# Kernel optimization log

Hardware: AMD Instinct MI355X
Metric: run time of the kernel (lower is better)

Reference implementation:

```python
import jax, jax.numpy as jnp
import numpy as np

B, L, IN, OUT = 32, 2048, 192, 2
H, N2, NL = 512, 32, 4  # hidden_dim, d_state//2 complex modes, num_layers


def setup_inputs() -> dict:
    key = jax.random.key(0)
    ks = jax.random.split(key, 8)
    neural_input = jax.random.normal(ks[0], (B, L, IN), jnp.float32)
    W_in = jax.random.normal(ks[1], (IN, H), jnp.float32) / np.sqrt(IN)
    b_in = jnp.zeros((H,), jnp.float32)
    # S4D kernel params (stacked over layers)
    log_dt = jax.random.uniform(ks[2], (NL, H), jnp.float32, np.log(1e-3), np.log(1e-1))
    Cri = jax.random.normal(ks[3], (NL, H, N2, 2), jnp.float32)  # complex C as (re, im)
    log_A_real = jnp.full((NL, H, N2), np.log(0.5), jnp.float32)
    A_imag = jnp.broadcast_to(np.pi * jnp.arange(N2, dtype=np.float32), (NL, H, N2)).astype(jnp.float32)
    D = jax.random.normal(ks[4], (NL, H), jnp.float32)
    # position-wise output conv1x1 producing 2H channels for GLU
    conv_w = jax.random.normal(ks[5], (NL, 2 * H, H), jnp.float32) / np.sqrt(H)
    conv_b = jnp.zeros((NL, 2 * H), jnp.float32)
    W_out = jax.random.normal(ks[6], (H, OUT), jnp.float32) / np.sqrt(H)
    b_out = jnp.zeros((OUT,), jnp.float32)
    return dict(neural_input=neural_input, W_in=W_in, b_in=b_in, log_dt=log_dt,
                Cri=Cri, log_A_real=log_A_real, A_imag=A_imag, D=D,
                conv_w=conv_w, conv_b=conv_b, W_out=W_out, b_out=b_out)


def _s4d_layer(u, log_dt, Cri, log_A_real, A_imag, D, conv_w, conv_b):
    # u: (B, H, L)
    Lx = u.shape[-1]
    dt = jnp.exp(log_dt)[:, None]                       # (H, 1)
    C = Cri[..., 0] + 1j * Cri[..., 1]                  # (H, N2) complex
    A = -jnp.exp(log_A_real) + 1j * A_imag              # (H, N2)
    dtA = A * dt                                        # (H, N2)
    Ct = C * (jnp.exp(dtA) - 1.0) / A                   # (H, N2)
    # Vandermonde kernel: K[h, l] = 2 Re sum_n Ct[h,n] exp(dtA[h,n] * l)
    vand = jnp.exp(dtA[..., None] * jnp.arange(Lx))     # (H, N2, L) complex
    K = 2.0 * jnp.einsum('hn,hnl->hl', Ct, vand).real   # (H, L)
    # circular conv via FFT at length 2L (== linear conv, causal)
    k_f = jnp.fft.rfft(K, n=2 * Lx)
    u_f = jnp.fft.rfft(u, n=2 * Lx)
    y = jnp.fft.irfft(u_f * k_f, n=2 * Lx)[..., :Lx]    # (B, H, L)
    y = y + u * D[:, None]
    y = jax.nn.gelu(y, approximate=False)               # torch nn.GELU (erf)
    # conv1x1 to 2H channels + GLU over channel dim
    z = jnp.einsum('oh,bhl->bol', conv_w, y) + conv_b[None, :, None]
    a, b = jnp.split(z, 2, axis=1)
    return a * jax.nn.sigmoid(b)


def reference(neural_input, W_in, b_in, log_dt, Cri, log_A_real, A_imag, D,
              conv_w, conv_b, W_out, b_out):
    x = neural_input @ W_in + b_in          # (B, L, H)
    u = jnp.transpose(x, (0, 2, 1))         # (B, H, L) channels-first for SSM
    for i in range(NL):
        u = _s4d_layer(u, log_dt[i], Cri[i], log_A_real[i], A_imag[i],
                       D[i], conv_w[i], conv_b[i])
    y = jnp.transpose(u, (0, 2, 1))         # (B, L, H)
    return y @ W_out + b_out                # (B, L, OUT)
```

## Files before the change

kernel.cpp:

```cpp
#include <hip/hip_runtime.h>
#include <hip/hip_bf16.h>
#include <math.h>

#define BB 32
#define LL 2048
#define INP 192
#define OUTC 2
#define HH 512
#define NN2 32
#define NNL 4
#define TABB 32768

using short8 = __attribute__((ext_vector_type(8))) short;
using f32x4  = __attribute__((ext_vector_type(4))) float;
using f32x2  = __attribute__((ext_vector_type(2))) float;

struct u2x2 { uint2 a, b; };

__device__ __forceinline__ float sigmoidf_(float x) {
  return 1.0f / (1.0f + expf(-x));
}
__device__ __forceinline__ unsigned short bf16bits(float x) {
  __hip_bfloat16 b = __float2bfloat16(x);
  return __builtin_bit_cast(unsigned short, b);
}
__device__ __forceinline__ float bfval(unsigned short b) {
  unsigned int u = (unsigned int)b << 16;
  return __builtin_bit_cast(float, u);
}
__device__ __forceinline__ unsigned packsplit(float v) {
  unsigned short hb = bf16bits(v);
  unsigned short lb = bf16bits(v - bfval(hb));
  return ((unsigned)hb << 16) | (unsigned)lb;
}
__device__ __forceinline__ float gelu_fast(float x) {
  float s = x * 0.70710678118654752f;
  float ax = fabsf(s);
  float tt = 1.0f / fmaf(0.3275911f, ax, 1.0f);
  float p = fmaf(1.061405429f, tt, -1.453152027f);
  p = fmaf(p, tt, 1.421413741f);
  p = fmaf(p, tt, -0.284496736f);
  p = fmaf(p, tt, 0.254829592f);
  float e = __expf(-s * s);
  float er = 1.0f - p * tt * e;
  er = copysignf(er, s);
  return 0.5f * x * (1.0f + er);
}
__device__ __forceinline__ void gload16(const void* gsrc, void* ldst) {
  __builtin_amdgcn_global_load_lds(
      (const __attribute__((address_space(1))) void*)gsrc,
      (__attribute__((address_space(3))) void*)ldst, 16, 0, 0);
}

__global__ __launch_bounds__(256) void k_params(const float* __restrict__ log_dt,
                                                const float* __restrict__ Cri,
                                                const float* __restrict__ lAr,
                                                const float* __restrict__ Aim,
                                                float* __restrict__ P) {
  int idx = blockIdx.x * 256 + threadIdx.x;
  if (idx >= NNL * HH * NN2) return;
  float dt  = expf(log_dt[idx / NN2]);
  float Are = -expf(lAr[idx]);
  float Aimv = Aim[idx];
  float dre = Are * dt, dim = Aimv * dt;
  float er = expf(dre);
  float wrv = er * cosf(dim);
  float wiv = er * sinf(dim);
  float Er = wrv - 1.0f, Ei = wiv;
  float den = Are * Are + Aimv * Aimv;
  float Fr = (Er * Are + Ei * Aimv) / den;
  float Fi = (Ei * Are - Er * Aimv) / den;
  float Cre = Cri[idx * 2 + 0], Cim = Cri[idx * 2 + 1];
  P[idx * 4 + 0] = wrv;
  P[idx * 4 + 1] = wiv;
  P[idx * 4 + 2] = 2.0f * (Cre * Fr - Cim * Fi);
  P[idx * 4 + 3] = 2.0f * (Cre * Fi + Cim * Fr);
}

__global__ __launch_bounds__(64) void k_tables(const float* __restrict__ P,
                                               const float* __restrict__ Dp,
                                               char* __restrict__ Tab) {
  __shared__ float kk[32];
  int tid = threadIdx.x;
  int lh = blockIdx.x;
  char* tb = Tab + (size_t)lh * TABB;
  if (tid < 32) {
    int n = tid;
    const float4 pq = reinterpret_cast<const float4*>(P)[(size_t)lh * NN2 + n];
    float wr = pq.x, wi = pq.y, c2r = pq.z, c2i = pq.w;
    int mt = n >> 4;
    float pr = 1.0f, pi = 0.0f;
    for (int d = 0; d < 32; ++d) {
      {
        int t_ = 31 - d;
        int lane = ((t_ >> 3) << 4) + (n & 15);
        int j = t_ & 7;
        unsigned short hr = bf16bits(pr);
        unsigned short lr = bf16bits(pr - bfval(hr));
        unsigned short hi_ = bf16bits(pi);
        unsigned short li_ = bf16bits(pi - bfval(hi_));
        *(unsigned short*)(tb + (mt * 2 + 0) * 1024 + lane * 16 + j * 2) = hr;
        *(unsigned short*)(tb + (mt * 2 + 1) * 1024 + lane * 16 + j * 2) = hi_;
        *(unsigned short*)(tb + 4096 + (mt * 2 + 0) * 1024 + lane * 16 + j * 2) = lr;
        *(unsigned short*)(tb + 4096 + (mt * 2 + 1) * 1024 + lane * 16 + j * 2) = li_;
      }
      {
        int mtT = d >> 4;
        int lane = (((n & 15) >> 2) << 4) + (d & 15);
        int jre = n & 3, jim = (n & 3) + 4;
        unsigned short hr = bf16bits(pr);
        unsigned short lr = bf16bits(pr - bfval(hr));
        float nim = -pi;
        unsigned short hi_ = bf16bits(nim);
        unsigned short li_ = bf16bits(nim - bfval(hi_));
        char* bh = tb + 8192 + (mtT * 2 + mt) * 1024 + lane * 16;
        char* bl = tb + 12288 + (mtT * 2 + mt) * 1024 + lane * 16;
        *(unsigned short*)(bh + jre * 2) = hr;
        *(unsigned short*)(bh + jim * 2) = hi_;
        *(unsigned short*)(bl + jre * 2) = lr;
        *(unsigned short*)(bl + jim * 2) = li_;
      }
      float kp = c2r * pr - c2i * pi;
      #pragma unroll
      for (int k = 1; k < 32; k <<= 1) kp += __shfl_xor(kp, k, 32);
      if (n == 0) kk[d] = (d == 0) ? (kp + Dp[lh]) : kp;
      float nr = pr * wr - pi * wi;
      pi = pr * wi + pi * wr;
      pr = nr;
    }
    float w32r = pr, w32i = pi;
    float c2wr = c2r * wr - c2i * wi;
    float c2wi = c2r * wi + c2i * wr;
    int s = ((n >> 4) << 2) + (n & 3);
    int gg = (n & 15) >> 2;
    float pmr = 1.0f, pmi = 0.0f;
    for (int m = 0; m < 16; ++m) {
      float* q = (float*)(tb + 20480 + (size_t)((s * 64) + (gg * 16 + m)) * 24);
      q[0] = w32r; q[1] = w32i; q[2] = pmr; q[3] = pmi; q[4] = c2wr; q[5] = c2wi;
      float t2 = pmr * w32r - pmi * w32i;
      pmi = pmr * w32i + pmi * w32r;
      pmr = t2;
    }
  }
  __syncthreads();
  for (int idx = tid; idx < 1024; idx += 64) {
    int mt = idx >> 9, rem = idx & 511;
    int lane = rem >> 3, j = rem & 7;
    int tt = (mt << 4) + (lane & 15);
    int jf = ((lane >> 4) << 3) + j;
    float val = (jf <= tt) ? kk[tt - jf] : 0.0f;
    unsigned short hb = bf16bits(val);
    unsigned short lb = bf16bits(val - bfval(hb));
    *(unsigned short*)(tb + 16384 + mt * 1024 + lane * 16 + j * 2) = hb;
    *(unsigned short*)(tb + 18432 + mt * 1024 + lane * 16 + j * 2) = lb;
  }
}

__global__ __launch_bounds__(256) void k_tobf16(const float* __restrict__ src,
                                                __hip_bfloat16* __restrict__ dst,
                                                int n) {
  int i = (blockIdx.x * 256 + threadIdx.x) * 4;
  if (i >= n) return;
  float4 v = *reinterpret_cast<const float4*>(&src[i]);
  dst[i + 0] = __float2bfloat16(v.x);
  dst[i + 1] = __float2bfloat16(v.y);
  dst[i + 2] = __float2bfloat16(v.z);
  dst[i + 3] = __float2bfloat16(v.w);
}

__global__ __launch_bounds__(256) void k_splitx(const float* __restrict__ src,
                                                __hip_bfloat16* __restrict__ hi,
                                                __hip_bfloat16* __restrict__ lo,
                                                int n) {
  int i = (blockIdx.x * 256 + threadIdx.x) * 4;
  if (i >= n) return;
  float4 v = *reinterpret_cast<const float4*>(&src[i]);
  float vv[4] = {v.x, v.y, v.z, v.w};
  unsigned short hb[4], lb[4];
  #pragma unroll
  for (int j = 0; j < 4; ++j) {
    hb[j] = bf16bits(vv[j]);
    lb[j] = bf16bits(vv[j] - bfval(hb[j]));
  }
  *reinterpret_cast<uint2*>(hi + i) = make_uint2(
      (unsigned)hb[0] | ((unsigned)hb[1] << 16), (unsigned)hb[2] | ((unsigned)hb[3] << 16));
  *reinterpret_cast<uint2*>(lo + i) = make_uint2(
      (unsigned)lb[0] | ((unsigned)lb[1] << 16), (unsigned)lb[2] | ((unsigned)lb[3] << 16));
}

__global__ __launch_bounds__(256) void k_prepwt(const float* __restrict__ W,
                                                __hip_bfloat16* __restrict__ hi,
                                                __hip_bfloat16* __restrict__ lo) {
  int idx = blockIdx.x * 256 + threadIdx.x;
  if (idx >= HH * INP) return;
  int h = idx / INP, k = idx - h * INP;
  float v = W[(size_t)k * HH + h];
  unsigned short hb = bf16bits(v);
  hi[idx] = __builtin_bit_cast(__hip_bfloat16, hb);
  lo[idx] = __float2bfloat16(v - bfval(hb));
}

__global__ __launch_bounds__(256) void k_ingemm(const __hip_bfloat16* __restrict__ Xhi,
                                                const __hip_bfloat16* __restrict__ Xlo,
                                                const __hip_bfloat16* __restrict__ Wthi,
                                                const __hip_bfloat16* __restrict__ Wtlo,
                                                const float* __restrict__ bias,
                                                unsigned* __restrict__ Upk) {
  int lt = blockIdx.x * 128;
  int ht = blockIdx.y * 128;
  int b  = blockIdx.z;
  int t = threadIdx.x;
  int wid = t >> 6, lane = t & 63;
  int wrow = wid >> 1, wcol = wid & 1;
  int l15 = lane & 15, g = lane >> 4;

  const short* Xh = (const short*)Xhi + (size_t)b * LL * INP;
  const short* Xl = (const short*)Xlo + (size_t)b * LL * INP;
  const short* Bh = (const short*)Wthi;
  const short* Bl = (const short*)Wtlo;

  f32x4 acc[4][4];
  #pragma unroll
  for (int m = 0; m < 4; ++m)
    #pragma unroll
    for (int n = 0; n < 4; ++n) acc[m][n] = f32x4{0.f, 0.f, 0.f, 0.f};

  int lbase = lt + wrow * 64 + l15;
  int hbase = ht + wcol * 64 + l15;

  #pragma unroll
  for (int ks = 0; ks < 6; ++ks) {
    int k0 = ks * 32 + 8 * g;
    short8 ah[4], al[4], bh[4], bl[4];
    #pragma unroll
    for (int m = 0; m < 4; ++m) {
      size_t off = (size_t)(lbase + m * 16) * INP + k0;
      ah[m] = *reinterpret_cast<const short8*>(Xh + off);
      al[m] = *reinterpret_cast<const short8*>(Xl + off);
    }
    #pragma unroll
    for (int n = 0; n < 4; ++n) {
      size_t off = (size_t)(hbase + n * 16) * INP + k0;
      bh[n] = *reinterpret_cast<const short8*>(Bh + off);
      bl[n] = *reinterpret_cast<const short8*>(Bl + off);
    }
    #pragma unroll
    for (int m = 0; m < 4; ++m)
      #pragma unroll
      for (int n = 0; n < 4; ++n) {
        acc[m][n] = __builtin_amdgcn_mfma_f32_16x16x32_bf16(ah[m], bh[n], acc[m][n], 0, 0, 0);
        acc[m][n] = __builtin_amdgcn_mfma_f32_16x16x32_bf16(ah[m], bl[n], acc[m][n], 0, 0, 0);
        acc[m][n] = __builtin_amdgcn_mfma_f32_16x16x32_bf16(al[m], bh[n], acc[m][n], 0, 0, 0);
      }
  }

  #pragma unroll
  for (int n = 0; n < 4; ++n) {
    int h = hbase + n * 16;
    float bv = bias[h];
    size_t rowoff = ((size_t)b * HH + h) * LL;
    #pragma unroll
    for (int m = 0; m < 4; ++m) {
      int l0 = lt + wrow * 64 + m * 16 + g * 4;
      uint4 o;
      o.x = packsplit(acc[m][n][0] + bv);
      o.y = packsplit(acc[m][n][1] + bv);
      o.z = packsplit(acc[m][n][2] + bv);
      o.w = packsplit(acc[m][n][3] + bv);
      *reinterpret_cast<uint4*>(Upk + rowoff + l0) = o;
    }
  }
}

__global__ __launch_bounds__(256) void k_scan(const unsigned* __restrict__ Upk,
                                              short* __restrict__ Ybt,
                                              const char* __restrict__ Tab) {
  __shared__ __align__(16) char smem[16384];
  int t = threadIdx.x;
  int lane = t & 63;
  int wid = t >> 6;
  int row = __builtin_amdgcn_readfirstlane(blockIdx.x * 4 + wid);
  int h = row & (HH - 1);
  const char* tb = Tab + (size_t)h * TABB;
  const unsigned* urow = Upk + (size_t)row * LL;
  int g = lane >> 4, m = lane & 15;

  short8 uh[4], ul[4];
  #pragma unroll
  for (int c0 = 0; c0 < 4; ++c0) {
    int off = 512 * c0 + 32 * m + 8 * g;
    uint4 pa = *reinterpret_cast<const uint4*>(urow + off);
    uint4 pb = *reinterpret_cast<const uint4*>(urow + off + 4);
    unsigned p[8] = {pa.x, pa.y, pa.z, pa.w, pb.x, pb.y, pb.z, pb.w};
    unsigned hw[4], lw[4];
    #pragma unroll
    for (int w = 0; w < 4; ++w) {
      unsigned p0 = p[2 * w], p1 = p[2 * w + 1];
      hw[w] = (p1 & 0xFFFF0000u) | (p0 >> 16);
      lw[w] = (p1 << 16) | (p0 & 0x0000FFFFu);
    }
    uh[c0] = __builtin_bit_cast(short8, make_uint4(hw[0], hw[1], hw[2], hw[3]));
    ul[c0] = __builtin_bit_cast(short8, make_uint4(lw[0], lw[1], lw[2], lw[3]));
  }

  short8 afh[2][4], afl[2][4];
  #pragma unroll
  for (int mt = 0; mt < 2; ++mt) {
    f32x4 Z[2][4];
    #pragma unroll
    for (int reim = 0; reim < 2; ++reim) {
      short8 whi = *reinterpret_cast<const short8*>(tb + (mt * 2 + reim) * 1024 + lane * 16);
      short8 wlo = *reinterpret_cast<const short8*>(tb + 4096 + (mt * 2 + reim) * 1024 + lane * 16);
      #pragma unroll
      for (int c0 = 0; c0 < 4; ++c0) {
        f32x4 z = {0.f, 0.f, 0.f, 0.f};
        z = __builtin_amdgcn_mfma_f32_16x16x32_bf16(whi, uh[c0], z, 0, 0, 0);
        z = __builtin_amdgcn_mfma_f32_16x16x32_bf16(whi, ul[c0], z, 0, 0, 0);
        z = __builtin_amdgcn_mfma_f32_16x16x32_bf16(wlo, uh[c0], z, 0, 0, 0);
        Z[reim][c0] = z;
      }
    }
    #pragma unroll
    for (int i = 0; i < 4; ++i) {
      int s = mt * 4 + i;
      const char* plb = tb + 20480 + (size_t)(s * 64 + lane) * 24;
      f32x2 w32 = *reinterpret_cast<const f32x2*>(plb);
      f32x2 w32m = *reinterpret_cast<const f32x2*>(plb + 8);
      f32x2 c2w = *reinterpret_cast<const f32x2*>(plb + 16);
      float r1r = w32[0], r1i = w32[1];
      float r2r = r1r * r1r - r1i * r1i, r2i = 2.f * r1r * r1i;
      float r4r = r2r * r2r - r2i * r2i, r4i = 2.f * r2r * r2i;
      float r8r = r4r * r4r - r4i * r4i, r8i = 2.f * r4r * r4i;
      float w16r = r8r * r8r - r8i * r8i, w16i = 2.f * r8r * r8i;

      float Er[4], Ei[4], Tr[4], Ti[4];
      #pragma unroll
      for (int c0 = 0; c0 < 4; ++c0) {
        float Pr = Z[0][c0][i], Pi = Z[1][c0][i];
        {
          float qr = __shfl_up(Pr, 1u, 16), qi = __shfl_up(Pi, 1u, 16);
          if (m < 1) { qr = 0.f; qi = 0.f; }
          Pr = fmaf(r1r, qr, fmaf(-r1i, qi, Pr));
          Pi = fmaf(r1r, qi, fmaf(r1i, qr, Pi));
        }
        {
          float qr = __shfl_up(Pr, 2u, 16), qi = __shfl_up(Pi, 2u, 16);
          if (m < 2) { qr = 0.f; qi = 0.f; }
          Pr = fmaf(r2r, qr, fmaf(-r2i, qi, Pr));
          Pi = fmaf(r2r, qi, fmaf(r2i, qr, Pi));
        }
        {
          float qr = __shfl_up(Pr, 4u, 16), qi = __shfl_up(Pi, 4u, 16);
          if (m < 4) { qr = 0.f; qi = 0.f; }
          Pr = fmaf(r4r, qr, fmaf(-r4i, qi, Pr));
          Pi = fmaf(r4r, qi, fmaf(r4i, qr, Pi));
        }
        {
          float qr = __shfl_up(Pr, 8u, 16), qi = __shfl_up(Pi, 8u, 16);
          if (m < 8) { qr = 0.f; qi = 0.f; }
          Pr = fmaf(r8r, qr, fmaf(-r8i, qi, Pr));
          Pi = fmaf(r8r, qi, fmaf(r8i, qr, Pi));
        }
        float eqr = __shfl_up(Pr, 1u, 16), eqi = __shfl_up(Pi, 1u, 16);
        if (m == 0) { eqr = 0.f; eqi = 0.f; }
        Er[c0] = eqr; Ei[c0] = eqi;
        Tr[c0] = __shfl(Pr, 15, 16);
        Ti[c0] = __shfl(Pi, 15, 16);
      }
      float C1r = Tr[0], C1i = Ti[0];
      float C2r = fmaf(w16r, C1r, fmaf(-w16i, C1i, Tr[1]));
      float C2i = fmaf(w16r, C1i, fmaf(w16i, C1r, Ti[1]));
      float C3r = fmaf(w16r, C2r, fmaf(-w16i, C2i, Tr[2]));
      float C3i = fmaf(w16r, C2i, fmaf(w16i, C2r, Ti[2]));
      float Cr[4] = {0.f, C1r, C2r, C3r};
      float Ci[4] = {0.f, C1i, C2i, C3i};
      #pragma unroll
      for (int c0 = 0; c0 < 4; ++c0) {
        float Erc = fmaf(w32m[0], Cr[c0], fmaf(-w32m[1], Ci[c0], Er[c0]));
        float Eic = fmaf(w32m[0], Ci[c0], fmaf(w32m[1], Cr[c0], Ei[c0]));
        float ar = c2w[0] * Erc - c2w[1] * Eic;
        float ai = c2w[0] * Eic + c2w[1] * Erc;
        unsigned short hr = bf16bits(ar);
        afh[mt][c0][i] = (short)hr;
        afl[mt][c0][i] = (short)bf16bits(ar - bfval(hr));
        unsigned short hi2 = bf16bits(ai);
        afh[mt][c0][4 + i] = (short)hi2;
        afl[mt][c0][4 + i] = (short)bf16bits(ai - bfval(hi2));
      }
    }
  }

  f32x4 y[2][4];
  #pragma unroll
  for (int mtT = 0; mtT < 2; ++mtT) {
    short8 fh = *reinterpret_cast<const short8*>(tb + 16384 + mtT * 1024 + lane * 16);
    short8 fl = *reinterpret_cast<const short8*>(tb + 18432 + mtT * 1024 + lane * 16);
    short8 wch0 = *reinterpret_cast<const short8*>(tb + 8192 + (mtT * 2 + 0) * 1024 + lane * 16);
    short8 wcl0 = *reinterpret_cast<const short8*>(tb + 12288 + (mtT * 2 + 0) * 1024 + lane * 16);
    short8 wch1 = *reinterpret_cast<const short8*>(tb + 8192 + (mtT * 2 + 1) * 1024 + lane * 16);
    short8 wcl1 = *reinterpret_cast<const short8*>(tb + 12288 + (mtT * 2 + 1) * 1024 + lane * 16);
    #pragma unroll
    for (int c0 = 0; c0 < 4; ++c0) {
      f32x4 acc = {0.f, 0.f, 0.f, 0.f};
      acc = __builtin_amdgcn_mfma_f32_16x16x32_bf16(fh, uh[c0], acc, 0, 0, 0);
      acc = __builtin_amdgcn_mfma_f32_16x16x32_bf16(fh, ul[c0], acc, 0, 0, 0);
      acc = __builtin_amdgcn_mfma_f32_16x16x32_bf16(fl, uh[c0], acc, 0, 0, 0);
      acc = __builtin_amdgcn_mfma_f32_16x16x32_bf16(wch0, afh[0][c0], acc, 0, 0, 0);
      acc = __builtin_amdgcn_mfma_f32_16x16x32_bf16(wch0, afl[0][c0], acc, 0, 0, 0);
      acc = __builtin_amdgcn_mfma_f32_16x16x32_bf16(wcl0, afh[0][c0], acc, 0, 0, 0);
      acc = __builtin_amdgcn_mfma_f32_16x16x32_bf16(wch1, afh[1][c0], acc, 0, 0, 0);
      acc = __builtin_amdgcn_mfma_f32_16x16x32_bf16(wch1, afl[1][c0], acc, 0, 0, 0);
      acc = __builtin_amdgcn_mfma_f32_16x16x32_bf16(wcl1, afh[1][c0], acc, 0, 0, 0);
      y[mtT][c0] = acc;
    }
  }

  #pragma unroll
  for (int mtT = 0; mtT < 2; ++mtT)
    #pragma unroll
    for (int c0 = 0; c0 < 4; ++c0) {
      int eb = 512 * c0 + 32 * m + 16 * mtT + 4 * g;
      f32x4 vv = y[mtT][c0];
      unsigned short bv[4];
      bv[0] = bf16bits(gelu_fast(vv[0]));
      bv[1] = bf16bits(gelu_fast(vv[1]));
      bv[2] = bf16bits(gelu_fast(vv[2]));
      bv[3] = bf16bits(gelu_fast(vv[3]));
      #pragma unroll
      for (int k = 0; k < 4; ++k) {
        int l = eb + k;
        *(short*)(smem + ((l * 8 + wid * 2) ^ (((l >> 5) & 7) << 3))) = (short)bv[k];
      }
    }
  __syncthreads();
  #pragma unroll
  for (int i = 0; i < 8; ++i) {
    int l = t + 256 * i;
    uint2 v = *reinterpret_cast<const uint2*>(smem + ((l * 8) ^ (((l >> 5) & 7) << 3)));
    *reinterpret_cast<uint2*>(Ybt + ((size_t)blockIdx.x * 2048 + l) * 4) = v;
  }
}

__global__ __launch_bounds__(256) void k_conv(const short* __restrict__ Ybt,
                                              const __hip_bfloat16* __restrict__ CWb,
                                              const float* __restrict__ CB,
                                              unsigned* __restrict__ Upk) {
  __shared__ short Alds[128 * 64];
  int lt = blockIdx.x * 128;
  int ot = blockIdx.y * 64;
  int b  = blockIdx.z;
  int t = threadIdx.x;
  int wid = t >> 6, lane = t & 63;
  int wr = wid >> 1, wc = wid & 1;
  int l15 = lane & 15, l4 = lane >> 4;
  f32x4 zero = {0.f, 0.f, 0.f, 0.f};
  f32x4 accA[2][4], accG[2][4];
  #pragma unroll
  for (int m = 0; m < 2; ++m)
    #pragma unroll
    for (int n = 0; n < 4; ++n) { accA[m][n] = zero; accG[m][n] = zero; }

  const short* Yb = Ybt + (size_t)b * 128 * 2048 * 4;
  const char* Wb = (const char*)CWb;

  for (int kt = 0; kt < HH; kt += 64) {
    #pragma unroll
    for (int it = 0; it < 4; ++it) {
      int d = 16 * (t + 256 * it);
      int rowl = d >> 7, cb = d & 127;
      int orow = (rowl < 64) ? (ot + rowl) : (448 + ot + rowl);
      gload16(Wb + (size_t)orow * 1024 + kt * 2 + (cb ^ ((rowl & 7) << 4)),
              (char*)Alds + d);
    }
    short8 bfrag[2][4];
    #pragma unroll
    for (int ks = 0; ks < 2; ++ks)
      #pragma unroll
      for (int n = 0; n < 4; ++n) {
        int l = lt + wc * 64 + n * 16 + l15;
        int octg = (kt >> 3) + ks * 4 + l4;
        const short* p0 = Yb + ((size_t)(2 * octg) * 2048 + l) * 4;
        uint2 A = *reinterpret_cast<const uint2*>(p0);
        uint2 B2 = *reinterpret_cast<const uint2*>(p0 + 8192);
        bfrag[ks][n] = __builtin_bit_cast(short8, u2x2{A, B2});
      }
    __syncthreads();
    #pragma unroll
    for (int ks = 0; ks < 2; ++ks) {
      short8 af[4];
      #pragma unroll
      for (int m = 0; m < 4; ++m) {
        int mrow = ((m < 2) ? (wr * 32 + m * 16) : (64 + wr * 32 + (m - 2) * 16)) + l15;
        int colb = (ks * 64 + 16 * l4) ^ ((mrow & 7) << 4);
        af[m] = *reinterpret_cast<const short8*>((const char*)Alds + mrow * 128 + colb);
      }
      #pragma unroll
      for (int m = 0; m < 2; ++m)
        #pragma unroll
        for (int n = 0; n < 4; ++n) {
          accA[m][n] = __builtin_amdgcn_mfma_f32_16x16x32_bf16(af[m], bfrag[ks][n], accA[m][n], 0, 0, 0);
          accG[m][n] = __builtin_amdgcn_mfma_f32_16x16x32_bf16(af[m + 2], bfrag[ks][n], accG[m][n], 0, 0, 0);
        }
    }
    __syncthreads();
  }
  #pragma unroll
  for (int m = 0; m < 2; ++m) {
    #pragma unroll
    for (int r = 0; r < 4; ++r) {
      int rowl = wr * 32 + m * 16 + l4 * 4 + r;
      float ba = CB[ot + rowl];
      float bg = CB[512 + ot + rowl];
      size_t rowoff = ((size_t)b * HH + ot + rowl) * LL + lt + wc * 64;
      #pragma unroll
      for (int n = 0; n < 4; ++n) {
        float a = accA[m][n][r] + ba;
        float gg = accG[m][n][r] + bg;
        Upk[rowoff + n * 16 + l15] = packsplit(a * sigmoidf_(gg));
      }
    }
  }
}

__global__ __launch_bounds__(256) void k_outgemm(const unsigned* __restrict__ Upk,
                                                 const float* __restrict__ Wo,
                                                 const float* __restrict__ bo,
                                                 float* __restrict__ out) {
  int bl = blockIdx.x * 256 + threadIdx.x;
  int b = bl >> 11, l = bl & (LL - 1);
  float a0 = 0.0f, a1 = 0.0f;
  const unsigned* up = Upk + (size_t)b * HH * LL + l;
  #pragma unroll 4
  for (int h = 0; h < HH; ++h) {
    unsigned u = up[(size_t)h * LL];
    float v = bfval((unsigned short)(u >> 16)) + bfval((unsigned short)(u & 0xFFFFu));
    a0 = fmaf(v, Wo[h * 2 + 0], a0);
    a1 = fmaf(v, Wo[h * 2 + 1], a1);
  }
  out[(size_t)bl * 2 + 0] = a0 + bo[0];
  out[(size_t)bl * 2 + 1] = a1 + bo[1];
}

extern "C" void kernel_launch(void* const* d_in, const int* in_sizes, int n_in,
                              void* d_out, int out_size, void* d_ws, size_t ws_size,
                              hipStream_t stream) {
  const float* X      = (const float*)d_in[0];
  const float* Win    = (const float*)d_in[1];
  const float* bin    = (const float*)d_in[2];
  const float* log_dt = (const float*)d_in[3];
  const float* Cri    = (const float*)d_in[4];
  const float* lAr    = (const float*)d_in[5];
  const float* Aim    = (const float*)d_in[6];
  const float* Dp     = (const float*)d_in[7];
  const float* CW     = (const float*)d_in[8];
  const float* CB     = (const float*)d_in[9];
  const float* Wo     = (const float*)d_in[10];
  const float* bo     = (const float*)d_in[11];
  float* out = (float*)d_out;

  const size_t Pfloats   = (size_t)NNL * HH * NN2 * 4;
  const size_t CWfloats  = (size_t)NNL * 2 * HH * HH / 2;
  const size_t Tabfloats = (size_t)NNL * HH * (TABB / 4);
  const size_t Wtfloats  = (size_t)HH * INP;
  const size_t Xnf       = (size_t)BB * LL * INP;
  const size_t HL        = (size_t)HH * LL;

  float* P = (float*)d_ws;
  __hip_bfloat16* CWb = (__hip_bfloat16*)(P + Pfloats);
  char* Tab = (char*)(P + Pfloats + CWfloats);
  __hip_bfloat16* Wthi = (__hip_bfloat16*)(P + Pfloats + CWfloats + Tabfloats);
  __hip_bfloat16* Wtlo = Wthi + Wtfloats;
  __hip_bfloat16* Xhi  = (__hip_bfloat16*)(P + Pfloats + CWfloats + Tabfloats + Wtfloats);
  __hip_bfloat16* Xlo  = Xhi + Xnf;
  size_t head = Pfloats + CWfloats + Tabfloats + Wtfloats + Xnf;

  size_t ws_floats = ws_size / sizeof(float);
  size_t avail = (ws_floats > head) ? (ws_floats - head) : 0;
  int G = (int)(avail / (HL + HL / 2));
  if (G >= 32) G = 32;
  else if (G >= 16) G = 16;
  else if (G >= 8) G = 8;
  else if (G >= 4) G = 4;
  else if (G >= 2) G = 2;
  else G = 1;

  unsigned* Upk = (unsigned*)(P + head);
  short* Ybt = (short*)(Upk + (size_t)G * HL);

  k_params<<<(NNL * HH * NN2 + 255) / 256, 256, 0, stream>>>(log_dt, Cri, lAr, Aim, P);
  k_tables<<<NNL * HH, 64, 0, stream>>>(P, Dp, Tab);
  k_tobf16<<<(NNL * 2 * HH * HH) / 1024, 256, 0, stream>>>(CW, CWb, NNL * 2 * HH * HH);
  k_prepwt<<<(HH * INP + 255) / 256, 256, 0, stream>>>(Win, Wthi, Wtlo);
  k_splitx<<<(int)(Xnf / 1024), 256, 0, stream>>>(X, Xhi, Xlo, (int)Xnf);

  for (int b0 = 0; b0 < BB; b0 += G) {
    int g = (BB - b0 < G) ? (BB - b0) : G;
    k_ingemm<<<dim3(LL / 128, HH / 128, g), 256, 0, stream>>>(
        Xhi + (size_t)b0 * LL * INP, Xlo + (size_t)b0 * LL * INP, Wthi, Wtlo, bin, Upk);
    for (int layer = 0; layer < NNL; ++layer) {
      k_scan<<<g * (HH / 4), 256, 0, stream>>>(
          Upk, Ybt, Tab + (size_t)layer * HH * TABB);
      k_conv<<<dim3(LL / 128, HH / 64, g), 256, 0, stream>>>(
          Ybt, CWb + (size_t)layer * 2 * HH * HH, CB + (size_t)layer * 2 * HH, Upk);
    }
    k_outgemm<<<g * LL / 256, 256, 0, stream>>>(
        Upk, Wo, bo, out + (size_t)b0 * LL * OUTC);
  }
}
```

Measured before the change: 1.212 ms.

## Shrink scan tables and alias X split buffer with Ybt to allow full batch

The per-channel scan table drops its redundant per-lane copies of w32 and c2w: those now live in a small per-group record loaded as one float4, so the table size falls and the scan kernel reads fewer bytes. Workspace layout changes so the bf16 split of the input shares memory with the Ybt buffer. This lets all 32 batches be processed in a single group when the workspace is large enough, which cuts repeated launches. The input split now runs per batch group inside the loop. The aliasing depends on splitx and ingemm finishing before scan writes Ybt, which holds because they run in order on one stream.

```diff
diff --git a/kernel.cpp b/kernel.cpp
--- a/kernel.cpp
+++ b/kernel.cpp
@@ -9,7 +9,7 @@
 #define HH 512
 #define NN2 32
 #define NNL 4
-#define TABB 32768
+#define TABB 25088
 
 using short8 = __attribute__((ext_vector_type(8))) short;
 using f32x4  = __attribute__((ext_vector_type(4))) float;
@@ -133,10 +133,12 @@
     float c2wi = c2r * wi + c2i * wr;
     int s = ((n >> 4) << 2) + (n & 3);
     int gg = (n & 15) >> 2;
+    float* q2 = (float*)(tb + 24576 + (size_t)(s * 4 + gg) * 16);
+    q2[0] = w32r; q2[1] = w32i; q2[2] = c2wr; q2[3] = c2wi;
     float pmr = 1.0f, pmi = 0.0f;
     for (int m = 0; m < 16; ++m) {
-      float* q = (float*)(tb + 20480 + (size_t)((s * 64) + (gg * 16 + m)) * 24);
-      q[0] = w32r; q[1] = w32i; q[2] = pmr; q[3] = pmi; q[4] = c2wr; q[5] = c2wi;
+      float* q = (float*)(tb + 20480 + (size_t)((s * 64) + (gg * 16 + m)) * 8);
+      q[0] = pmr; q[1] = pmi;
       float t2 = pmr * w32r - pmi * w32i;
       pmi = pmr * w32i + pmi * w32r;
       pmr = t2;
@@ -323,11 +325,10 @@
     #pragma unroll
     for (int i = 0; i < 4; ++i) {
       int s = mt * 4 + i;
-      const char* plb = tb + 20480 + (size_t)(s * 64 + lane) * 24;
-      f32x2 w32 = *reinterpret_cast<const f32x2*>(plb);
-      f32x2 w32m = *reinterpret_cast<const f32x2*>(plb + 8);
-      f32x2 c2w = *reinterpret_cast<const f32x2*>(plb + 16);
-      float r1r = w32[0], r1i = w32[1];
+      f32x2 w32m = *reinterpret_cast<const f32x2*>(tb + 20480 + (size_t)(s * 64 + lane) * 8);
+      float4 cc = *reinterpret_cast<const float4*>(tb + 24576 + (size_t)(s * 4 + g) * 16);
+      float r1r = cc.x, r1i = cc.y;
+      f32x2 c2w = {cc.z, cc.w};
       float r2r = r1r * r1r - r1i * r1i, r2i = 2.f * r1r * r1i;
       float r4r = r2r * r2r - r2i * r2i, r4i = 2.f * r2r * r2i;
       float r8r = r4r * r4r - r4i * r4i, r8i = 2.f * r4r * r4i;
@@ -570,33 +571,52 @@
   char* Tab = (char*)(P + Pfloats + CWfloats);
   __hip_bfloat16* Wthi = (__hip_bfloat16*)(P + Pfloats + CWfloats + Tabfloats);
   __hip_bfloat16* Wtlo = Wthi + Wtfloats;
-  __hip_bfloat16* Xhi  = (__hip_bfloat16*)(P + Pfloats + CWfloats + Tabfloats + Wtfloats);
-  __hip_bfloat16* Xlo  = Xhi + Xnf;
-  size_t head = Pfloats + CWfloats + Tabfloats + Wtfloats + Xnf;
+  size_t base = Pfloats + CWfloats + Tabfloats + Wtfloats;
 
   size_t ws_floats = ws_size / sizeof(float);
-  size_t avail = (ws_floats > head) ? (ws_floats - head) : 0;
-  int G = (int)(avail / (HL + HL / 2));
-  if (G >= 32) G = 32;
-  else if (G >= 16) G = 16;
-  else if (G >= 8) G = 8;
-  else if (G >= 4) G = 4;
-  else if (G >= 2) G = 2;
-  else G = 1;
-
-  unsigned* Upk = (unsigned*)(P + head);
-  short* Ybt = (short*)(Upk + (size_t)G * HL);
+
+  size_t upk32 = (size_t)32 * HL;
+  size_t ybt32 = (size_t)32 * HL / 2;
+  size_t region32 = (Xnf > ybt32) ? Xnf : ybt32;
+
+  int G;
+  unsigned* Upk;
+  short* Ybt;
+  __hip_bfloat16 *Xhi, *Xlo;
+
+  if (ws_floats >= base + upk32 + region32) {
+    G = 32;
+    Upk = (unsigned*)(P + base);
+    float* region = P + base + upk32;
+    Xhi = (__hip_bfloat16*)region;
+    Xlo = Xhi + Xnf;
+    Ybt = (short*)region;
+  } else {
+    Xhi = (__hip_bfloat16*)(P + base);
+    Xlo = Xhi + Xnf;
+    size_t head = base + Xnf;
+    size_t avail = (ws_floats > head) ? (ws_floats - head) : 0;
+    G = (int)(avail / (HL + HL / 2));
+    if (G >= 16) G = 16;
+    else if (G >= 8) G = 8;
+    else if (G >= 4) G = 4;
+    else if (G >= 2) G = 2;
+    else G = 1;
+    Upk = (unsigned*)(P + head);
+    Ybt = (short*)(Upk + (size_t)G * HL);
+  }
 
   k_params<<<(NNL * HH * NN2 + 255) / 256, 256, 0, stream>>>(log_dt, Cri, lAr, Aim, P);
   k_tables<<<NNL * HH, 64, 0, stream>>>(P, Dp, Tab);
   k_tobf16<<<(NNL * 2 * HH * HH) / 1024, 256, 0, stream>>>(CW, CWb, NNL * 2 * HH * HH);
   k_prepwt<<<(HH * INP + 255) / 256, 256, 0, stream>>>(Win, Wthi, Wtlo);
-  k_splitx<<<(int)(Xnf / 1024), 256, 0, stream>>>(X, Xhi, Xlo, (int)Xnf);
 
   for (int b0 = 0; b0 < BB; b0 += G) {
     int g = (BB - b0 < G) ? (BB - b0) : G;
+    k_splitx<<<(int)((size_t)g * LL * INP / 1024), 256, 0, stream>>>(
+        X + (size_t)b0 * LL * INP, Xhi, Xlo, (int)((size_t)g * LL * INP));
     k_ingemm<<<dim3(LL / 128, HH / 128, g), 256, 0, stream>>>(
-        Xhi + (size_t)b0 * LL * INP, Xlo + (size_t)b0 * LL * INP, Wthi, Wtlo, bin, Upk);
+        Xhi, Xlo, Wthi, Wtlo, bin, Upk);
     for (int layer = 0; layer < NNL; ++layer) {
       k_scan<<<g * (HH / 4), 256, 0, stream>>>(
           Upk, Ybt, Tab + (size_t)layer * HH * TABB);
```

Measured after the change: 1.090 ms. -10.0%, faster.
